# Optimization experiments

Hardware: AMD Instinct MI355X
Metric: run time of the kernel (lower is better)

Reference implementation:

```python
import math
import jax, jax.numpy as jnp
import numpy as np

HEADS = 16

def setup_inputs() -> dict:
    key = jax.random.key(0)
    k1, k2, k3, k4, k5 = jax.random.split(key, 5)
    B, T, W = 2, 2048, 1024
    x = jax.random.normal(k1, (B, T, W), dtype=jnp.float32)
    # Linear params stored as [in, out] for x @ W + b
    W_qkv = jax.random.normal(k2, (W, 3 * W), dtype=jnp.float32) / math.sqrt(W)
    b_qkv = jnp.zeros((3 * W,), dtype=jnp.float32)
    W_proj = jax.random.normal(k3, (W, W), dtype=jnp.float32) / math.sqrt(W)
    b_proj = jnp.zeros((W,), dtype=jnp.float32)
    return {"x": x, "W_qkv": W_qkv, "b_qkv": b_qkv, "W_proj": W_proj, "b_proj": b_proj}


def reference(x, W_qkv, b_qkv, W_proj, b_proj):
    B, T, width = x.shape
    heads = HEADS
    attn_ch = width // heads  # == (3*width) // heads // 3
    scale = 1.0 / math.sqrt(math.sqrt(attn_ch))

    qkv = x @ W_qkv + b_qkv                      # [B, T, 3W]
    qkv = qkv.reshape(B, T, heads, 3 * attn_ch)
    q, k, v = jnp.split(qkv, 3, axis=-1)          # each [B, T, H, C]

    # manual attention with float32 softmax over full score matrix
    weight = jnp.einsum('bthc,bshc->bhts', q * scale, k * scale)
    weight = jax.nn.softmax(weight.astype(jnp.float32), axis=-1).astype(qkv.dtype)
    out = jnp.einsum('bhts,bshc->bthc', weight, v)  # [B, T, H, C]

    # adaptive position-wise weight from Q-K mean interaction
    k_mean = k.mean(axis=1)                                   # [B, H, C]
    interaction = jnp.einsum('bthc,bhc->bth', q * scale, k_mean * scale)
    pos = interaction.sum(axis=-1)                            # [B, T]
    mn = pos.min(axis=1, keepdims=True)
    mx = pos.max(axis=1, keepdims=True)
    aw = (pos - mn) / (mx - mn + 1e-6)                        # [B, T]

    out = aw[:, :, None, None] * out
    out = out.reshape(B, T, width)
    return out @ W_proj + b_proj
```

## Files before the change

### kernel.cpp

```cpp
#include <hip/hip_runtime.h>
#include <hip/hip_bf16.h>


#define LOG2E 1.4426950408889634f

typedef float f32x4 __attribute__((ext_vector_type(4)));
typedef short bf16x8 __attribute__((ext_vector_type(8)));

__device__ __forceinline__ unsigned short f2bf(float f) {
  union { float f; unsigned int u; } v; v.f = f;
  unsigned int r = v.u + 0x7fffu + ((v.u >> 16) & 1u);
  return (unsigned short)(r >> 16);
}
__device__ __forceinline__ float bf2f(unsigned short h) {
  union { unsigned int u; float f; } v; v.u = ((unsigned int)h) << 16;
  return v.f;
}
__device__ __forceinline__ unsigned int pk_bf16(float a, float b) {
  union { __hip_bfloat162 h; unsigned int u; } v;
  v.h = __float22bfloat162_rn(make_float2(a, b));
  return v.u;
}

__global__ __launch_bounds__(256) void conv_split(
    const float* __restrict__ in, unsigned short* __restrict__ hi,
    unsigned short* __restrict__ lo) {
  size_t base = ((size_t)blockIdx.x * 256 + threadIdx.x) * 8;
  float4 v0 = *(const float4*)&in[base];
  float4 v1 = *(const float4*)&in[base + 4];
  float f[8] = {v0.x, v0.y, v0.z, v0.w, v1.x, v1.y, v1.z, v1.w};
  unsigned int hw[4], lw[4];
#pragma unroll
  for (int p = 0; p < 4; ++p) {
    float a = f[2 * p], b = f[2 * p + 1];
    unsigned short ha = f2bf(a), hb = f2bf(b);
    unsigned short la = f2bf(a - bf2f(ha)), lb = f2bf(b - bf2f(hb));
    hw[p] = (unsigned int)ha | ((unsigned int)hb << 16);
    lw[p] = (unsigned int)la | ((unsigned int)lb << 16);
  }
  uint4 H = {hw[0], hw[1], hw[2], hw[3]};
  uint4 L = {lw[0], lw[1], lw[2], lw[3]};
  *(uint4*)&hi[base] = H;
  *(uint4*)&lo[base] = L;
}

__global__ __launch_bounds__(256) void conv_split_T(
    const float* __restrict__ in, unsigned short* __restrict__ hi,
    unsigned short* __restrict__ lo, int K, int N) {
  __shared__ float t[32][33];
  const int n0 = blockIdx.x * 32, k0 = blockIdx.y * 32;
  const int r = threadIdx.x >> 3, c4 = (threadIdx.x & 7) * 4;
  float4 v = *(const float4*)&in[(size_t)(k0 + r) * N + n0 + c4];
  t[r][c4 + 0] = v.x; t[r][c4 + 1] = v.y; t[r][c4 + 2] = v.z; t[r][c4 + 3] = v.w;
  __syncthreads();
  unsigned int hw[2], lw[2];
#pragma unroll
  for (int p = 0; p < 2; ++p) {
    float a = t[c4 + 2 * p][r], b = t[c4 + 2 * p + 1][r];
    unsigned short ha = f2bf(a), hb = f2bf(b);
    unsigned short la = f2bf(a - bf2f(ha)), lb = f2bf(b - bf2f(hb));
    hw[p] = (unsigned int)ha | ((unsigned int)hb << 16);
    lw[p] = (unsigned int)la | ((unsigned int)lb << 16);
  }
  size_t o = (size_t)(n0 + r) * K + k0 + c4;
  *(uint2*)&hi[o] = make_uint2(hw[0], hw[1]);
  *(uint2*)&lo[o] = make_uint2(lw[0], lw[1]);
}

__global__ __launch_bounds__(256, 2) void gemm_mfma_split(
    const unsigned short* __restrict__ Ah, const unsigned short* __restrict__ Al,
    const unsigned short* __restrict__ Bh, const unsigned short* __restrict__ Bl,
    const float* __restrict__ bias, float* __restrict__ C,
    int M, int N, int K) {
  __shared__ __align__(16) unsigned short lds[2][16384];

  const int tid = threadIdx.x;
  const int w = tid >> 6, l = tid & 63;
  const int lc = l & 15, lr = l >> 4;
  const int wr = w >> 1, wc = w & 1;
  const int m0 = blockIdx.y * 128, n0 = blockIdx.x * 128;

  f32x4 acc[4][4];
#pragma unroll
  for (int mi = 0; mi < 4; ++mi)
#pragma unroll
    for (int ni = 0; ni < 4; ++ni) acc[mi][ni] = (f32x4){0.f, 0.f, 0.f, 0.f};

  const unsigned short* src = (w == 0) ? Ah : (w == 1) ? Al : (w == 2) ? Bh : Bl;
  const int rowbase = (w < 2) ? m0 : n0;
  const int lrow = l >> 2, lkk = (l & 3) * 8;

  const int NT = K / 32;
  int buf = 0;

#define STAGE(B_, KT_)                                                         \
  {                                                                            \
    unsigned short* dst = lds[B_] + w * 4096;                                  \
    _Pragma("unroll") for (int c = 0; c < 8; ++c) {                            \
      const unsigned short* g =                                                \
          src + (size_t)(rowbase + c * 16 + lrow) * K + (KT_) + lkk;           \
      __builtin_amdgcn_global_load_lds(                                        \
          (const __attribute__((address_space(1))) unsigned int*)g,            \
          (__attribute__((address_space(3))) unsigned int*)(dst + c * 512),    \
          16, 0, 0);                                                           \
    }                                                                          \
  }

  STAGE(0, 0);
  asm volatile("s_waitcnt vmcnt(0)");
  __syncthreads();

  for (int t = 0; t < NT; ++t) {
    if (t + 1 < NT) STAGE(buf ^ 1, (t + 1) * 32);

    const unsigned short* bp = lds[buf];
    bf16x8 ah[4], al[4], bh[4], bl[4];
#pragma unroll
    for (int mi = 0; mi < 4; ++mi) {
      int ro = (wr * 64 + mi * 16 + lc) * 32 + lr * 8;
      ah[mi] = *(const bf16x8*)&bp[ro];
      al[mi] = *(const bf16x8*)&bp[4096 + ro];
    }
#pragma unroll
    for (int ni = 0; ni < 4; ++ni) {
      int co = (wc * 64 + ni * 16 + lc) * 32 + lr * 8;
      bh[ni] = *(const bf16x8*)&bp[8192 + co];
      bl[ni] = *(const bf16x8*)&bp[12288 + co];
    }

    __builtin_amdgcn_s_setprio(1);
#pragma unroll
    for (int mi = 0; mi < 4; ++mi)
#pragma unroll
      for (int ni = 0; ni < 4; ++ni) {
        acc[mi][ni] = __builtin_amdgcn_mfma_f32_16x16x32_bf16(ah[mi], bh[ni], acc[mi][ni], 0, 0, 0);
        acc[mi][ni] = __builtin_amdgcn_mfma_f32_16x16x32_bf16(ah[mi], bl[ni], acc[mi][ni], 0, 0, 0);
        acc[mi][ni] = __builtin_amdgcn_mfma_f32_16x16x32_bf16(al[mi], bh[ni], acc[mi][ni], 0, 0, 0);
      }
    __builtin_amdgcn_s_setprio(0);

    __syncthreads();
    buf ^= 1;
  }
#undef STAGE

#pragma unroll
  for (int mi = 0; mi < 4; ++mi)
#pragma unroll
    for (int r = 0; r < 4; ++r) {
      int row = m0 + wr * 64 + mi * 16 + lr * 4 + r;
#pragma unroll
      for (int ni = 0; ni < 4; ++ni) {
        int col = n0 + wc * 64 + ni * 16 + lc;
        C[(size_t)row * N + col] = acc[mi][ni][r] + bias[col];
      }
    }
}

__global__ __launch_bounds__(256) void convert_kernel(
    const float* __restrict__ qkv,
    unsigned short* __restrict__ Qh, unsigned short* __restrict__ Ql,
    unsigned short* __restrict__ Ktg, unsigned short* __restrict__ Vtg) {
  const int stile = blockIdx.x, bh = blockIdx.y;
  const int b = bh >> 4, h = bh & 15;
  const int tid = threadIdx.x;
  const int s = tid >> 2;
  const int cg = (tid & 3) << 4;
  const int t = stile * 64 + s;
  const float* row = qkv + (size_t)(b * 2048 + t) * 3072 + h * 192;
  const float QS = 0.125f * LOG2E;

  __shared__ unsigned short vs[64][72];

  {
    unsigned int* qh32 = (unsigned int*)(Qh + ((size_t)bh * 2048 + t) * 64 + cg);
    unsigned int* ql32 = (unsigned int*)(Ql + ((size_t)bh * 2048 + t) * 64 + cg);
#pragma unroll
    for (int j = 0; j < 4; ++j) {
      float4 v = *(const float4*)&row[cg + j * 4];
      float f[4] = {v.x * QS, v.y * QS, v.z * QS, v.w * QS};
      unsigned short hh[4], llo[4];
#pragma unroll
      for (int e = 0; e < 4; ++e) {
        hh[e] = f2bf(f[e]);
        llo[e] = f2bf(f[e] - bf2f(hh[e]));
      }
      qh32[j * 2 + 0] = (unsigned int)hh[0] | ((unsigned int)hh[1] << 16);
      qh32[j * 2 + 1] = (unsigned int)hh[2] | ((unsigned int)hh[3] << 16);
      ql32[j * 2 + 0] = (unsigned int)llo[0] | ((unsigned int)llo[1] << 16);
      ql32[j * 2 + 1] = (unsigned int)llo[2] | ((unsigned int)llo[3] << 16);
    }
  }
  {
    unsigned int* kt32 = (unsigned int*)(Ktg + (size_t)(bh * 32 + stile) * 4096);
    const int sw = (s & 7) << 4;
#pragma unroll
    for (int j = 0; j < 4; ++j) {
      float4 v = *(const float4*)&row[64 + cg + j * 4];
      float f[4] = {v.x, v.y, v.z, v.w};
#pragma unroll
      for (int p = 0; p < 2; ++p) {
        int c0 = cg + j * 4 + p * 2;
        int byte = (s * 128 + c0 * 2) ^ sw;
        kt32[byte >> 2] = (unsigned int)f2bf(f[p * 2]) |
                          ((unsigned int)f2bf(f[p * 2 + 1]) << 16);
      }
    }
  }
#pragma unroll
  for (int j = 0; j < 4; ++j) {
    float4 v = *(const float4*)&row[128 + cg + j * 4];
    vs[s][cg + j * 4 + 0] = f2bf(v.x);
    vs[s][cg + j * 4 + 1] = f2bf(v.y);
    vs[s][cg + j * 4 + 2] = f2bf(v.z);
    vs[s][cg + j * 4 + 3] = f2bf(v.w);
  }
  __syncthreads();
  {
    const int c = tid >> 2;
    const int sb = (tid & 3) << 4;
    unsigned int* vt32 = (unsigned int*)(Vtg + (size_t)(bh * 32 + stile) * 4096);
    const int sw = (c & 7) << 4;
#pragma unroll
    for (int p = 0; p < 8; ++p) {
      int ss = sb + p * 2;
      unsigned int wv = (unsigned int)vs[ss][c] | ((unsigned int)vs[ss + 1][c] << 16);
      int byte = (c * 128 + ss * 2) ^ sw;
      vt32[byte >> 2] = wv;
    }
  }
}

__global__ __launch_bounds__(256, 4) void attn_mfma(
    const unsigned short* __restrict__ Qh, const unsigned short* __restrict__ Ql,
    const unsigned short* __restrict__ Ktg, const unsigned short* __restrict__ Vtg,
    const float* __restrict__ aw,
    unsigned short* __restrict__ A2h, unsigned short* __restrict__ A2l) {
  const int qt = blockIdx.x, bh = blockIdx.y;
  const int b = bh >> 4, h = bh & 15;
  const int tid = threadIdx.x;
  const int w = tid >> 6, l = tid & 63;
  const int lc = l & 15, lr = l >> 4;

  __shared__ __align__(16) unsigned short ldsKV[2][8192];
  __shared__ __align__(16) unsigned short ldsP[4096];
  unsigned short* Pl = ldsP + w * 1024;
  unsigned int* Plw = (unsigned int*)Pl;

  const int q0 = qt * 64 + w * 16;
  bf16x8 qh0, qh1, ql0, ql1;
  {
    size_t base = ((size_t)bh * 2048 + q0 + lc) * 64 + lr * 8;
    qh0 = *(const bf16x8*)&Qh[base];
    qh1 = *(const bf16x8*)&Qh[base + 32];
    ql0 = *(const bf16x8*)&Ql[base];
    ql1 = *(const bf16x8*)&Ql[base + 32];
  }

  int kidx0[4], kidx1[4];
#pragma unroll
  for (int st = 0; st < 4; ++st) {
    int row = st * 16 + lc;
    int sw = (row & 7) << 4;
    kidx0[st] = ((row * 128 + lr * 16) ^ sw) >> 1;
    kidx1[st] = ((row * 128 + 64 + lr * 16) ^ sw) >> 1;
  }
  int pww[4][2];
  {
    int sw = (lc & 7) << 4;
#pragma unroll
    for (int st = 0; st < 4; ++st)
#pragma unroll
      for (int rp = 0; rp < 2; ++rp)
        pww[st][rp] = ((lc * 128 + st * 32 + lr * 8 + rp * 4) ^ sw) >> 2;
  }

  f32x4 o[4];
  float m = -1e30f, lsum = 0.f;
#pragma unroll
  for (int ct = 0; ct < 4; ++ct) o[ct] = (f32x4){0.f, 0.f, 0.f, 0.f};

  const unsigned short* gsrc =
      ((w < 2) ? Ktg : Vtg) + (size_t)bh * 32 * 4096 + (w & 1) * 2048 + l * 8;
  unsigned short* ldst0 = &ldsKV[0][(w >> 1) * 4096 + (w & 1) * 2048];
  unsigned short* ldst1 = &ldsKV[1][(w >> 1) * 4096 + (w & 1) * 2048];

#define STAGE_KV(DST_, T_)                                                     \
  {                                                                            \
    const unsigned short* g = gsrc + (size_t)(T_) * 4096;                      \
    _Pragma("unroll") for (int i = 0; i < 4; ++i) {                            \
      __builtin_amdgcn_global_load_lds(                                        \
          (const __attribute__((address_space(1))) unsigned int*)(g + i * 512),\
          (__attribute__((address_space(3))) unsigned int*)((DST_) + i * 512), \
          16, 0, 0);                                                           \
    }                                                                          \
  }

  STAGE_KV(ldst0, 0);
  asm volatile("s_waitcnt vmcnt(0)");
  __syncthreads();

  int buf = 0;
  for (int kvt = 0; kvt < 32; ++kvt) {
    if (kvt + 1 < 32) STAGE_KV(buf ? ldst0 : ldst1, kvt + 1);

    const unsigned short* KT = &ldsKV[buf][0];
    const unsigned short* VT = &ldsKV[buf][4096];

    f32x4 sacc[4];
    __builtin_amdgcn_s_setprio(1);
#pragma unroll
    for (int st = 0; st < 4; ++st) {
      bf16x8 k0 = *(const bf16x8*)&KT[kidx0[st]];
      bf16x8 k1 = *(const bf16x8*)&KT[kidx1[st]];
      f32x4 acc = (f32x4){0.f, 0.f, 0.f, 0.f};
      acc = __builtin_amdgcn_mfma_f32_16x16x32_bf16(k0, qh0, acc, 0, 0, 0);
      acc = __builtin_amdgcn_mfma_f32_16x16x32_bf16(k1, qh1, acc, 0, 0, 0);
      acc = __builtin_amdgcn_mfma_f32_16x16x32_bf16(k0, ql0, acc, 0, 0, 0);
      acc = __builtin_amdgcn_mfma_f32_16x16x32_bf16(k1, ql1, acc, 0, 0, 0);
      sacc[st] = acc;
    }
    __builtin_amdgcn_s_setprio(0);

    float pmax = fmaxf(fmaxf(fmaxf(sacc[0][0], sacc[0][1]), fmaxf(sacc[0][2], sacc[0][3])),
                       fmaxf(fmaxf(sacc[1][0], sacc[1][1]), fmaxf(sacc[1][2], sacc[1][3])));
    pmax = fmaxf(pmax,
           fmaxf(fmaxf(fmaxf(sacc[2][0], sacc[2][1]), fmaxf(sacc[2][2], sacc[2][3])),
                 fmaxf(fmaxf(sacc[3][0], sacc[3][1]), fmaxf(sacc[3][2], sacc[3][3]))));
    if (__any(pmax > m)) {
      float pm = fmaxf(pmax, __shfl_xor(pmax, 16));
      pm = fmaxf(pm, __shfl_xor(pm, 32));
      float mn = fmaxf(m, pm);
      float corr = exp2f(m - mn);
      m = mn;
      lsum *= corr;
#pragma unroll
      for (int r = 0; r < 4; ++r) {
        float cq = __shfl(corr, lr * 4 + r);
        o[0][r] *= cq; o[1][r] *= cq; o[2][r] *= cq; o[3][r] *= cq;
      }
    }

#pragma unroll
    for (int st = 0; st < 4; ++st)
#pragma unroll
      for (int r = 0; r < 4; ++r)
        sacc[st][r] = exp2f(sacc[st][r] - m);
#pragma unroll
    for (int st = 0; st < 4; ++st)
      lsum += (sacc[st][0] + sacc[st][1]) + (sacc[st][2] + sacc[st][3]);

#pragma unroll
    for (int st = 0; st < 4; ++st) {
      Plw[pww[st][0]] = pk_bf16(sacc[st][0], sacc[st][1]);
      Plw[pww[st][1]] = pk_bf16(sacc[st][2], sacc[st][3]);
    }

    bf16x8 pa0 = *(const bf16x8*)&Pl[kidx0[0]];
    bf16x8 pa1 = *(const bf16x8*)&Pl[kidx1[0]];

    __builtin_amdgcn_s_setprio(1);
#pragma unroll
    for (int ct = 0; ct < 4; ++ct) {
      bf16x8 v0 = *(const bf16x8*)&VT[kidx0[ct]];
      bf16x8 v1 = *(const bf16x8*)&VT[kidx1[ct]];
      o[ct] = __builtin_amdgcn_mfma_f32_16x16x32_bf16(pa0, v0, o[ct], 0, 0, 0);
      o[ct] = __builtin_amdgcn_mfma_f32_16x16x32_bf16(pa1, v1, o[ct], 0, 0, 0);
    }
    __builtin_amdgcn_s_setprio(0);
    __syncthreads();
    buf ^= 1;
  }
#undef STAGE_KV

  lsum += __shfl_xor(lsum, 16);
  lsum += __shfl_xor(lsum, 32);
  float inv = 1.0f / lsum;
#pragma unroll
  for (int r = 0; r < 4; ++r) {
    int t = q0 + lr * 4 + r;
    float sc = aw[b * 2048 + t] * __shfl(inv, lr * 4 + r);
    size_t off = (size_t)(b * 2048 + t) * 1024 + h * 64 + lc;
#pragma unroll
    for (int ct = 0; ct < 4; ++ct) {
      float v = o[ct][r] * sc;
      unsigned short hh = f2bf(v);
      A2h[off + ct * 16] = hh;
      A2l[off + ct * 16] = f2bf(v - bf2f(hh));
    }
  }
}

__global__ __launch_bounds__(256) void kmean_part(
    const unsigned short* __restrict__ Ktg, float* __restrict__ kmp) {
  const int bh = blockIdx.x, seg = blockIdx.y;
  const int c = threadIdx.x & 63, sub = threadIdx.x >> 6;
  const int tile = seg * 4 + sub;
  const unsigned short* kt = Ktg + (size_t)(bh * 32 + tile) * 4096;
  float sum = 0.f;
#pragma unroll 8
  for (int s = 0; s < 64; ++s) {
    int sidx = ((s * 128 + c * 2) ^ ((s & 7) << 4)) >> 1;
    sum += bf2f(kt[sidx]);
  }
  __shared__ float red[4][64];
  red[sub][c] = sum;
  __syncthreads();
  if (sub == 0)
    kmp[(size_t)(bh * 8 + seg) * 64 + c] =
        red[0][c] + red[1][c] + red[2][c] + red[3][c];
}

__global__ __launch_bounds__(256) void pos_kernel(
    const unsigned short* __restrict__ Qh, const unsigned short* __restrict__ Ql,
    const float* __restrict__ kmp, float* __restrict__ pos) {
  __shared__ float kms[1024];
  int blk = blockIdx.x;
  int b = (blk * 4) >> 11;
  for (int i = threadIdx.x; i < 1024; i += 256) {
    int h = i >> 6, cc = i & 63;
    float s = 0.f;
#pragma unroll
    for (int seg = 0; seg < 8; ++seg)
      s += kmp[(size_t)((b * 16 + h) * 8 + seg) * 64 + cc];
    kms[i] = s * (1.0f / 2048.0f) * (1.0f / LOG2E);
  }
  __syncthreads();
  int w = threadIdx.x >> 6, lane = threadIdx.x & 63;
  int row = blk * 4 + w;
  int t = row & 2047;
  float p = 0.f;
#pragma unroll
  for (int h = 0; h < 16; ++h) {
    size_t idx = ((size_t)(b * 16 + h) * 2048 + t) * 64 + lane;
    p = fmaf(bf2f(Qh[idx]) + bf2f(Ql[idx]), kms[h * 64 + lane], p);
  }
#pragma unroll
  for (int off = 32; off; off >>= 1) p += __shfl_xor(p, off, 64);
  if (lane == 0) pos[row] = p;
}

__global__ __launch_bounds__(1024) void aw_kernel(const float* __restrict__ pos,
                                                  float* __restrict__ aw) {
  int b = blockIdx.x, tid = threadIdx.x;
  float p0 = pos[b * 2048 + tid], p1 = pos[b * 2048 + 1024 + tid];
  float mn = fminf(p0, p1), mx = fmaxf(p0, p1);
#pragma unroll
  for (int off = 32; off; off >>= 1) {
    mn = fminf(mn, __shfl_xor(mn, off, 64));
    mx = fmaxf(mx, __shfl_xor(mx, off, 64));
  }
  __shared__ float smn[16], smx[16];
  int wave = tid >> 6, lane = tid & 63;
  if (lane == 0) { smn[wave] = mn; smx[wave] = mx; }
  __syncthreads();
  if (tid < 64) {
    mn = (lane < 16) ? smn[lane] : 3.0e38f;
    mx = (lane < 16) ? smx[lane] : -3.0e38f;
#pragma unroll
    for (int off = 8; off; off >>= 1) {
      mn = fminf(mn, __shfl_xor(mn, off, 64));
      mx = fmaxf(mx, __shfl_xor(mx, off, 64));
    }
    if (lane == 0) { smn[0] = mn; smx[0] = mx; }
  }
  __syncthreads();
  float MN = smn[0], inv = 1.0f / (smx[0] - MN + 1e-6f);
  aw[b * 2048 + tid] = (p0 - MN) * inv;
  aw[b * 2048 + 1024 + tid] = (p1 - MN) * inv;
}

extern "C" void kernel_launch(void* const* d_in, const int* in_sizes, int n_in,
                              void* d_out, int out_size, void* d_ws, size_t ws_size,
                              hipStream_t stream) {
  const float* x      = (const float*)d_in[0];
  const float* W_qkv  = (const float*)d_in[1];
  const float* b_qkv  = (const float*)d_in[2];
  const float* W_proj = (const float*)d_in[3];
  const float* b_proj = (const float*)d_in[4];
  float* out = (float*)d_out;

  char* wsb = (char*)d_ws;
  unsigned short* xh  = (unsigned short*)wsb;
  unsigned short* xl  = xh + 4194304;
  unsigned short* A2h = (unsigned short*)wsb;
  unsigned short* A2l = A2h + 4194304;
  float* qkv_f = (float*)(wsb + 16777216);
  unsigned short* Wqh = (unsigned short*)(wsb + 67108864);
  unsigned short* Wql = Wqh + 3145728;
  unsigned short* Qh  = (unsigned short*)(wsb + 67108864);
  unsigned short* Ql  = Qh + 4194304;
  unsigned short* Ktg = Ql + 4194304;
  unsigned short* Vtg = Ktg + 4194304;
  unsigned short* Wph = (unsigned short*)(wsb + 100663296);
  unsigned short* Wpl = Wph + 1048576;
  float* kmp = (float*)(wsb + 104857600);
  float* pos = kmp + 16384;
  float* aw  = pos + 4096;

  conv_split<<<2048, 256, 0, stream>>>(x, xh, xl);
  conv_split_T<<<dim3(96, 32), 256, 0, stream>>>(W_qkv, Wqh, Wql, 1024, 3072);
  conv_split_T<<<dim3(32, 32), 256, 0, stream>>>(W_proj, Wph, Wpl, 1024, 1024);
  gemm_mfma_split<<<dim3(24, 32), 256, 0, stream>>>(xh, xl, Wqh, Wql, b_qkv,
                                                    qkv_f, 4096, 3072, 1024);
  convert_kernel<<<dim3(32, 32), 256, 0, stream>>>(qkv_f, Qh, Ql, Ktg, Vtg);
  kmean_part<<<dim3(32, 8), 256, 0, stream>>>(Ktg, kmp);
  pos_kernel<<<1024, 256, 0, stream>>>(Qh, Ql, kmp, pos);
  aw_kernel<<<2, 1024, 0, stream>>>(pos, aw);
  attn_mfma<<<dim3(32, 32), 256, 0, stream>>>(Qh, Ql, Ktg, Vtg, aw, A2h, A2l);
  gemm_mfma_split<<<dim3(8, 32), 256, 0, stream>>>(A2h, A2l, Wph, Wpl, b_proj,
                                                   out, 4096, 1024, 1024);
}
```

Measured before the change: 330.0 us.

## Fuse QKV GEMM epilogue with bf16 split and K/V transpose; lazy softmax rescale

Replaces the QKV GEMM plus separate convert kernel with a single GEMM whose epilogue writes the scaled Q hi/lo split and the swizzled transposed K and V tiles directly. This drops the fp32 qkv round trip through global memory and one kernel launch, but the epilogue now does scattered 2-byte stores. In the attention kernel, P is written to LDS with 64-bit stores instead of two 32-bit stores. The online-softmax rescale is skipped unless the running max grows by more than 8 in log2 units, which cuts rescale work but allows exp2 values up to 256 and so changes rounding.

```diff
diff --git a/kernel.cpp b/kernel.cpp
--- a/kernel.cpp
+++ b/kernel.cpp
@@ -157,76 +157,132 @@
     }
 }
 
-__global__ __launch_bounds__(256) void convert_kernel(
-    const float* __restrict__ qkv,
+__global__ __launch_bounds__(256, 2) void gemm_qkv_fused(
+    const unsigned short* __restrict__ Ah, const unsigned short* __restrict__ Al,
+    const unsigned short* __restrict__ Bh, const unsigned short* __restrict__ Bl,
+    const float* __restrict__ bias,
     unsigned short* __restrict__ Qh, unsigned short* __restrict__ Ql,
     unsigned short* __restrict__ Ktg, unsigned short* __restrict__ Vtg) {
-  const int stile = blockIdx.x, bh = blockIdx.y;
-  const int b = bh >> 4, h = bh & 15;
+  const int M = 4096, N = 3072, K = 1024;
+  (void)M; (void)N;
+  __shared__ __align__(16) unsigned short lds[2][16384];
+
   const int tid = threadIdx.x;
-  const int s = tid >> 2;
-  const int cg = (tid & 3) << 4;
-  const int t = stile * 64 + s;
-  const float* row = qkv + (size_t)(b * 2048 + t) * 3072 + h * 192;
+  const int w = tid >> 6, l = tid & 63;
+  const int lc = l & 15, lr = l >> 4;
+  const int wr = w >> 1, wc = w & 1;
+  const int m0 = blockIdx.y * 128, n0 = blockIdx.x * 128;
+
+  f32x4 acc[4][4];
+#pragma unroll
+  for (int mi = 0; mi < 4; ++mi)
+#pragma unroll
+    for (int ni = 0; ni < 4; ++ni) acc[mi][ni] = (f32x4){0.f, 0.f, 0.f, 0.f};
+
+  const unsigned short* src = (w == 0) ? Ah : (w == 1) ? Al : (w == 2) ? Bh : Bl;
+  const int rowbase = (w < 2) ? m0 : n0;
+  const int lrow = l >> 2, lkk = (l & 3) * 8;
+
+  const int NT = K / 32;
+  int buf = 0;
+
+#define STAGEQ(B_, KT_)                                                        \
+  {                                                                            \
+    unsigned short* dst = lds[B_] + w * 4096;                                  \
+    _Pragma("unroll") for (int c = 0; c < 8; ++c) {                            \
+      const unsigned short* g =                                                \
+          src + (size_t)(rowbase + c * 16 + lrow) * K + (KT_) + lkk;           \
+      __builtin_amdgcn_global_load_lds(                                        \
+          (const __attribute__((address_space(1))) unsigned int*)g,            \
+          (__attribute__((address_space(3))) unsigned int*)(dst + c * 512),    \
+          16, 0, 0);                                                           \
+    }                                                                          \
+  }
+
+  STAGEQ(0, 0);
+  asm volatile("s_waitcnt vmcnt(0)");
+  __syncthreads();
+
+  for (int t = 0; t < NT; ++t) {
+    if (t + 1 < NT) STAGEQ(buf ^ 1, (t + 1) * 32);
+
+    const unsigned short* bp = lds[buf];
+    bf16x8 ah[4], al[4], bh[4], bl[4];
+#pragma unroll
+    for (int mi = 0; mi < 4; ++mi) {
+      int ro = (wr * 64 + mi * 16 + lc) * 32 + lr * 8;
+      ah[mi] = *(const bf16x8*)&bp[ro];
+      al[mi] = *(const bf16x8*)&bp[4096 + ro];
+    }
+#pragma unroll
+    for (int ni = 0; ni < 4; ++ni) {
+      int co = (wc * 64 + ni * 16 + lc) * 32 + lr * 8;
+      bh[ni] = *(const bf16x8*)&bp[8192 + co];
+      bl[ni] = *(const bf16x8*)&bp[12288 + co];
+    }
+
+    __builtin_amdgcn_s_setprio(1);
+#pragma unroll
+    for (int mi = 0; mi < 4; ++mi)
+#pragma unroll
+      for (int ni = 0; ni < 4; ++ni) {
+        acc[mi][ni] = __builtin_amdgcn_mfma_f32_16x16x32_bf16(ah[mi], bh[ni], acc[mi][ni], 0, 0, 0);
+        acc[mi][ni] = __builtin_amdgcn_mfma_f32_16x16x32_bf16(ah[mi], bl[ni], acc[mi][ni], 0, 0, 0);
+        acc[mi][ni] = __builtin_amdgcn_mfma_f32_16x16x32_bf16(al[mi], bh[ni], acc[mi][ni], 0, 0, 0);
+      }
+    __builtin_amdgcn_s_setprio(0);
+
+    __syncthreads();
+    buf ^= 1;
+  }
+#undef STAGEQ
+
   const float QS = 0.125f * LOG2E;
-
-  __shared__ unsigned short vs[64][72];
-
-  {
-    unsigned int* qh32 = (unsigned int*)(Qh + ((size_t)bh * 2048 + t) * 64 + cg);
-    unsigned int* ql32 = (unsigned int*)(Ql + ((size_t)bh * 2048 + t) * 64 + cg);
-#pragma unroll
-    for (int j = 0; j < 4; ++j) {
-      float4 v = *(const float4*)&row[cg + j * 4];
-      float f[4] = {v.x * QS, v.y * QS, v.z * QS, v.w * QS};
-      unsigned short hh[4], llo[4];
-#pragma unroll
-      for (int e = 0; e < 4; ++e) {
-        hh[e] = f2bf(f[e]);
-        llo[e] = f2bf(f[e] - bf2f(hh[e]));
-      }
-      qh32[j * 2 + 0] = (unsigned int)hh[0] | ((unsigned int)hh[1] << 16);
-      qh32[j * 2 + 1] = (unsigned int)hh[2] | ((unsigned int)hh[3] << 16);
-      ql32[j * 2 + 0] = (unsigned int)llo[0] | ((unsigned int)llo[1] << 16);
-      ql32[j * 2 + 1] = (unsigned int)llo[2] | ((unsigned int)llo[3] << 16);
-    }
-  }
-  {
-    unsigned int* kt32 = (unsigned int*)(Ktg + (size_t)(bh * 32 + stile) * 4096);
-    const int sw = (s & 7) << 4;
-#pragma unroll
-    for (int j = 0; j < 4; ++j) {
-      float4 v = *(const float4*)&row[64 + cg + j * 4];
-      float f[4] = {v.x, v.y, v.z, v.w};
-#pragma unroll
-      for (int p = 0; p < 2; ++p) {
-        int c0 = cg + j * 4 + p * 2;
-        int byte = (s * 128 + c0 * 2) ^ sw;
-        kt32[byte >> 2] = (unsigned int)f2bf(f[p * 2]) |
-                          ((unsigned int)f2bf(f[p * 2 + 1]) << 16);
-      }
-    }
-  }
-#pragma unroll
-  for (int j = 0; j < 4; ++j) {
-    float4 v = *(const float4*)&row[128 + cg + j * 4];
-    vs[s][cg + j * 4 + 0] = f2bf(v.x);
-    vs[s][cg + j * 4 + 1] = f2bf(v.y);
-    vs[s][cg + j * 4 + 2] = f2bf(v.z);
-    vs[s][cg + j * 4 + 3] = f2bf(v.w);
-  }
-  __syncthreads();
-  {
-    const int c = tid >> 2;
-    const int sb = (tid & 3) << 4;
-    unsigned int* vt32 = (unsigned int*)(Vtg + (size_t)(bh * 32 + stile) * 4096);
-    const int sw = (c & 7) << 4;
-#pragma unroll
-    for (int p = 0; p < 8; ++p) {
-      int ss = sb + p * 2;
-      unsigned int wv = (unsigned int)vs[ss][c] | ((unsigned int)vs[ss + 1][c] << 16);
-      int byte = (c * 128 + ss * 2) ^ sw;
-      vt32[byte >> 2] = wv;
+#pragma unroll
+  for (int ni = 0; ni < 4; ++ni) {
+    int col = n0 + wc * 64 + ni * 16 + lc;
+    int h = col / 192;
+    int rr = col - h * 192;
+    float bs = bias[col];
+    if (rr < 64) {
+      int c = rr;
+#pragma unroll
+      for (int mi = 0; mi < 4; ++mi)
+#pragma unroll
+        for (int r = 0; r < 4; ++r) {
+          int row = m0 + wr * 64 + mi * 16 + lr * 4 + r;
+          int bb = row >> 11, tl = row & 2047;
+          float v = (acc[mi][ni][r] + bs) * QS;
+          unsigned short hh = f2bf(v);
+          size_t off = ((size_t)(bb * 16 + h) * 2048 + tl) * 64 + c;
+          Qh[off] = hh;
+          Ql[off] = f2bf(v - bf2f(hh));
+        }
+    } else if (rr < 128) {
+      int c2 = (rr - 64) * 2;
+#pragma unroll
+      for (int mi = 0; mi < 4; ++mi)
+#pragma unroll
+        for (int r = 0; r < 4; ++r) {
+          int row = m0 + wr * 64 + mi * 16 + lr * 4 + r;
+          int bb = row >> 11, tl = row & 2047;
+          int s = tl & 63;
+          size_t base = (size_t)((bb * 16 + h) * 32 + (tl >> 6)) * 4096;
+          Ktg[base + (((s * 128 + c2) ^ ((s & 7) << 4)) >> 1)] =
+              f2bf(acc[mi][ni][r] + bs);
+        }
+    } else {
+      int cb = (rr - 128) * 128, csw = ((rr - 128) & 7) << 4;
+#pragma unroll
+      for (int mi = 0; mi < 4; ++mi)
+#pragma unroll
+        for (int r = 0; r < 4; ++r) {
+          int row = m0 + wr * 64 + mi * 16 + lr * 4 + r;
+          int bb = row >> 11, tl = row & 2047;
+          int s = tl & 63;
+          size_t base = (size_t)((bb * 16 + h) * 32 + (tl >> 6)) * 4096;
+          Vtg[base + (((cb + s * 2) ^ csw) >> 1)] = f2bf(acc[mi][ni][r] + bs);
+        }
     }
   }
 }
@@ -245,7 +301,7 @@
   __shared__ __align__(16) unsigned short ldsKV[2][8192];
   __shared__ __align__(16) unsigned short ldsP[4096];
   unsigned short* Pl = ldsP + w * 1024;
-  unsigned int* Plw = (unsigned int*)Pl;
+  uint2* Pl2 = (uint2*)Pl;
 
   const int q0 = qt * 64 + w * 16;
   bf16x8 qh0, qh1, ql0, ql1;
@@ -265,14 +321,12 @@
     kidx0[st] = ((row * 128 + lr * 16) ^ sw) >> 1;
     kidx1[st] = ((row * 128 + 64 + lr * 16) ^ sw) >> 1;
   }
-  int pww[4][2];
+  int pwd[4];
   {
     int sw = (lc & 7) << 4;
 #pragma unroll
     for (int st = 0; st < 4; ++st)
-#pragma unroll
-      for (int rp = 0; rp < 2; ++rp)
-        pww[st][rp] = ((lc * 128 + st * 32 + lr * 8 + rp * 4) ^ sw) >> 2;
+      pwd[st] = ((lc * 128 + st * 32 + lr * 8) ^ sw) >> 3;
   }
 
   f32x4 o[4];
@@ -327,7 +381,7 @@
     pmax = fmaxf(pmax,
            fmaxf(fmaxf(fmaxf(sacc[2][0], sacc[2][1]), fmaxf(sacc[2][2], sacc[2][3])),
                  fmaxf(fmaxf(sacc[3][0], sacc[3][1]), fmaxf(sacc[3][2], sacc[3][3]))));
-    if (__any(pmax > m)) {
+    if (__any(pmax > m + 8.0f)) {
       float pm = fmaxf(pmax, __shfl_xor(pmax, 16));
       pm = fmaxf(pm, __shfl_xor(pm, 32));
       float mn = fmaxf(m, pm);
@@ -352,8 +406,10 @@
 
 #pragma unroll
     for (int st = 0; st < 4; ++st) {
-      Plw[pww[st][0]] = pk_bf16(sacc[st][0], sacc[st][1]);
-      Plw[pww[st][1]] = pk_bf16(sacc[st][2], sacc[st][3]);
+      uint2 pv;
+      pv.x = pk_bf16(sacc[st][0], sacc[st][1]);
+      pv.y = pk_bf16(sacc[st][2], sacc[st][3]);
+      Pl2[pwd[st]] = pv;
     }
 
     bf16x8 pa0 = *(const bf16x8*)&Pl[kidx0[0]];
@@ -485,25 +541,23 @@
   unsigned short* xl  = xh + 4194304;
   unsigned short* A2h = (unsigned short*)wsb;
   unsigned short* A2l = A2h + 4194304;
-  float* qkv_f = (float*)(wsb + 16777216);
-  unsigned short* Wqh = (unsigned short*)(wsb + 67108864);
+  unsigned short* Wqh = (unsigned short*)(wsb + 16777216);
   unsigned short* Wql = Wqh + 3145728;
-  unsigned short* Qh  = (unsigned short*)(wsb + 67108864);
+  unsigned short* Qh  = (unsigned short*)(wsb + 33554432);
   unsigned short* Ql  = Qh + 4194304;
   unsigned short* Ktg = Ql + 4194304;
   unsigned short* Vtg = Ktg + 4194304;
-  unsigned short* Wph = (unsigned short*)(wsb + 100663296);
+  unsigned short* Wph = (unsigned short*)(wsb + 67108864);
   unsigned short* Wpl = Wph + 1048576;
-  float* kmp = (float*)(wsb + 104857600);
+  float* kmp = (float*)(wsb + 71303168);
   float* pos = kmp + 16384;
   float* aw  = pos + 4096;
 
   conv_split<<<2048, 256, 0, stream>>>(x, xh, xl);
   conv_split_T<<<dim3(96, 32), 256, 0, stream>>>(W_qkv, Wqh, Wql, 1024, 3072);
   conv_split_T<<<dim3(32, 32), 256, 0, stream>>>(W_proj, Wph, Wpl, 1024, 1024);
-  gemm_mfma_split<<<dim3(24, 32), 256, 0, stream>>>(xh, xl, Wqh, Wql, b_qkv,
-                                                    qkv_f, 4096, 3072, 1024);
-  convert_kernel<<<dim3(32, 32), 256, 0, stream>>>(qkv_f, Qh, Ql, Ktg, Vtg);
+  gemm_qkv_fused<<<dim3(24, 32), 256, 0, stream>>>(xh, xl, Wqh, Wql, b_qkv,
+                                                   Qh, Ql, Ktg, Vtg);
   kmean_part<<<dim3(32, 8), 256, 0, stream>>>(Ktg, kmp);
   pos_kernel<<<1024, 256, 0, stream>>>(Qh, Ql, kmp, pos);
   aw_kernel<<<2, 1024, 0, stream>>>(pos, aw);
```

Result: faster. 294.7 us (-10.7%).
